# Performance work log

Hardware: AMD Instinct MI355X
Metric: run time of the kernel (lower is better)

Reference implementation:

```python
import jax, jax.numpy as jnp
import numpy as np

D_MODEL = 1024
NUM_HEADS = 16
D_K = D_MODEL // NUM_HEADS
THETA = 10000.0
SEQ = 4096
BATCH = 1


def _rope(x, token_positions):
    # x: [b, h, s, d_k]; interleaved even/odd rotation as in the torch module
    kd = jnp.arange(0, D_K, 2, dtype=jnp.float32) / D_K          # [d_k/2]
    angles = token_positions[:, None].astype(jnp.float32) / (THETA ** kd)  # [s, d_k/2]
    cos_pos = jnp.cos(angles)
    sin_pos = jnp.sin(angles)
    x_even = x[..., 0::2]
    x_odd = x[..., 1::2]
    rot_even = x_even * cos_pos - x_odd * sin_pos
    rot_odd = x_even * sin_pos + x_odd * cos_pos
    rot = jnp.stack([rot_even, rot_odd], axis=-1)                # [..., d_k/2, 2]
    return rot.reshape(*x.shape[:-1], D_K)


def setup_inputs() -> dict:
    key = jax.random.key(0)
    k1, k2, k3 = jax.random.split(key, 3)
    std_qkv = np.sqrt(2.0 / (D_MODEL + 3 * D_MODEL))
    std_o = np.sqrt(2.0 / (D_MODEL + D_MODEL))
    x = jax.random.normal(k1, (BATCH, SEQ, D_MODEL), dtype=jnp.float32)
    Wqkv = jax.random.normal(k2, (3 * D_MODEL, D_MODEL), dtype=jnp.float32) * std_qkv
    Wo = jax.random.normal(k3, (D_MODEL, D_MODEL), dtype=jnp.float32) * std_o
    token_positions = jnp.arange(SEQ, dtype=jnp.int32)
    return {"x": x, "Wqkv": Wqkv, "Wo": Wo, "token_positions": token_positions}


def reference(x, Wqkv, Wo, token_positions):
    b, s, _ = x.shape
    qkv = jnp.einsum('bsd,ed->bse', x, Wqkv)                      # [b, s, 3*d_model]
    q, k, v = jnp.split(qkv, 3, axis=-1)

    def to_heads(t):
        return t.reshape(b, s, NUM_HEADS, D_K).transpose(0, 2, 1, 3)  # [b, h, s, d_k]

    q, k, v = to_heads(q), to_heads(k), to_heads(v)
    q = _rope(q, token_positions)
    k = _rope(k, token_positions)

    scores = jnp.einsum('bhqd,bhkd->bhqk', q, k) / jnp.sqrt(jnp.float32(D_K))
    mask = jnp.tril(jnp.ones((s, s), dtype=bool))
    scores = jnp.where(mask, scores, -jnp.inf)
    attn = jax.nn.softmax(scores, axis=-1)
    out = jnp.einsum('bhqk,bhkd->bhqd', attn, v)                  # [b, h, s, d_k]
    out = out.transpose(0, 2, 1, 3).reshape(b, s, D_MODEL)
    return jnp.einsum('bsd,ed->bse', out, Wo)
```

## Files before the change

### kernel.cpp

```cpp
#include <hip/hip_runtime.h>
#include <cstdint>

typedef unsigned short u16;
typedef __attribute__((ext_vector_type(8))) short short8;
typedef __attribute__((ext_vector_type(4))) float float4v;

__device__ __forceinline__ float bf2f(u16 u) {
    union { unsigned int i; float f; } v; v.i = ((unsigned int)u) << 16; return v.f;
}
__device__ __forceinline__ u16 f2bf(float f) {
    union { float f; unsigned int i; } v; v.f = f;
    unsigned int i = v.i;
    i += 0x7fffu + ((i >> 16) & 1u);
    return (u16)(i >> 16);
}
__device__ __forceinline__ unsigned cvt_pk_bf16(float lo, float hi) {
    unsigned r;
    asm("v_cvt_pk_bf16_f32 %0, %1, %2" : "=v"(r) : "v"(lo), "v"(hi));
    return r;
}
__device__ __forceinline__ void gl2lds16(const u16* g, u16* l) {
    __builtin_amdgcn_global_load_lds((const __attribute__((address_space(1))) void*)g,
                                     (__attribute__((address_space(3))) void*)l, 16, 0, 0);
}
__device__ __forceinline__ uint4 cvt8(const float* __restrict__ p) {
    float4 a = *(const float4*)p;
    float4 b = *(const float4*)(p + 4);
    u16 t[8] = {f2bf(a.x), f2bf(a.y), f2bf(a.z), f2bf(a.w),
                f2bf(b.x), f2bf(b.y), f2bf(b.z), f2bf(b.w)};
    return *(const uint4*)t;
}

__global__ void cvt_f32_bf16(const float* __restrict__ src, u16* __restrict__ dst, int n8) {
    int i = blockIdx.x * blockDim.x + threadIdx.x;
    if (i >= n8) return;
    *(uint4*)(dst + (size_t)i * 8) = cvt8(src + (size_t)i * 8);
}

__global__ void zero_f32(float* __restrict__ p, int n4) {
    int i = blockIdx.x * blockDim.x + threadIdx.x;
    if (i >= n4) return;
    float4 z = {0.f, 0.f, 0.f, 0.f};
    *(float4*)(p + (size_t)i * 4) = z;
}

__global__ __launch_bounds__(256) void gemm_bt(const u16* __restrict__ A,
                                               const u16* __restrict__ B,
                                               u16* __restrict__ C,
                                               int M, int N, int K) {
    __shared__ u16 As[128 * 32];
    __shared__ u16 Bs[128 * 32];
    const int tid  = threadIdx.x;
    const int wave = tid >> 6, lane = tid & 63;
    const int lg = lane >> 4, lr = lane & 15;
    const int bm = blockIdx.x * 128, bn = blockIdx.y * 128;
    const int wm = (wave & 1) * 64, wn = (wave >> 1) * 64;
    const int row = tid >> 2, co = (tid & 3) * 8;

    float4v acc[4][4] = {};

    for (int k0 = 0; k0 < K; k0 += 32) {
        gl2lds16(A + (size_t)(bm + row) * K + k0 + co,      As + tid * 8);
        gl2lds16(A + (size_t)(bm + 64 + row) * K + k0 + co, As + (tid + 256) * 8);
        gl2lds16(B + (size_t)(bn + row) * K + k0 + co,      Bs + tid * 8);
        gl2lds16(B + (size_t)(bn + 64 + row) * K + k0 + co, Bs + (tid + 256) * 8);
        __syncthreads();

        short8 af[4], bf[4];
        #pragma unroll
        for (int i = 0; i < 4; ++i)
            af[i] = *(const short8*)(As + (wm + i * 16 + lr) * 32 + lg * 8);
        #pragma unroll
        for (int j = 0; j < 4; ++j)
            bf[j] = *(const short8*)(Bs + (wn + j * 16 + lr) * 32 + lg * 8);
        #pragma unroll
        for (int i = 0; i < 4; ++i)
            #pragma unroll
            for (int j = 0; j < 4; ++j)
                acc[i][j] = __builtin_amdgcn_mfma_f32_16x16x32_bf16(af[i], bf[j], acc[i][j], 0, 0, 0);
        __syncthreads();
    }

    #pragma unroll
    for (int i = 0; i < 4; ++i)
        #pragma unroll
        for (int j = 0; j < 4; ++j)
            #pragma unroll
            for (int r = 0; r < 4; ++r) {
                int rw = bm + wm + i * 16 + lg * 4 + r;
                int cl = bn + wn + j * 16 + lr;
                C[(size_t)rw * N + cl] = f2bf(acc[i][j][r]);
            }
}

__global__ void rope_kernel(u16* __restrict__ qkv, const int* __restrict__ pos, int S) {
    int idx = blockIdx.x * blockDim.x + threadIdx.x;
    int s = idx >> 10;
    if (s >= S) return;
    int p    = idx & 1023;
    int part = p >> 9;
    int wi   = p & 511;
    int head = wi >> 5;
    int i    = wi & 31;
    int col  = part * 1024 + head * 64 + 2 * i;

    u16* ptr = qkv + (size_t)s * 3072 + col;
    ushort2 v = *(const ushort2*)ptr;
    float xe = bf2f(v.x), xo = bf2f(v.y);
    float freq = __expf(-(float)i * 0.2878231366242557f);
    float ang  = (float)pos[s] * freq;
    float sn = sinf(ang), cs = cosf(ang);
    float re = xe * cs - xo * sn;
    float ro = xe * sn + xo * cs;
    if (part == 0) { re *= 0.18033688011112042f; ro *= 0.18033688011112042f; }
    ushort2 o; o.x = f2bf(re); o.y = f2bf(ro);
    *(ushort2*)ptr = o;
}

__global__ __launch_bounds__(256) void transpose_v(const u16* __restrict__ qkv,
                                                   u16* __restrict__ VT) {
    __shared__ u16 T[64 * 65];
    const int h = blockIdx.y, s0 = blockIdx.x * 64;
    const int tid = threadIdx.x;
    #pragma unroll
    for (int i = 0; i < 2; ++i) {
        int seg = i * 256 + tid;
        int r = seg >> 3, c8 = (seg & 7) * 8;
        u16 tmp[8];
        *(uint4*)tmp = *(const uint4*)(qkv + (size_t)(s0 + r) * 3072 + 2048 + h * 64 + c8);
        #pragma unroll
        for (int j = 0; j < 8; ++j) T[r * 65 + c8 + j] = tmp[j];
    }
    __syncthreads();
    #pragma unroll
    for (int i = 0; i < 2; ++i) {
        int seg = i * 256 + tid;
        int d = seg >> 3, s8 = (seg & 7) * 8;
        u16 tmp[8];
        #pragma unroll
        for (int j = 0; j < 8; ++j) tmp[j] = T[(s8 + j) * 65 + d];
        *(uint4*)(VT + (size_t)(h * 64 + d) * 4096 + s0 + s8) = *(const uint4*)tmp;
    }
}

__global__ __launch_bounds__(512) void attn_kernel(const u16* __restrict__ qkv,
                                                   const u16* __restrict__ VT,
                                                   float* __restrict__ acc,
                                                   float* __restrict__ lac) {
    __shared__ u16 Ks[64 * 64];
    __shared__ u16 Vt[64 * 64];
    __shared__ u16 Ps[8][16 * 72];

    const int tid  = threadIdx.x;
    const int wave = tid >> 6, lane = tid & 63;
    const int lg = lane >> 4, lr = lane & 15;
    const int h  = blockIdx.y;
    const int z  = blockIdx.z;

    const int srow = tid >> 3;
    const int sg   = tid & 7;
    const int sco  = sg * 8;
    const int sldso = srow * 64 + ((sg ^ (srow & 7)) * 8);
    const int swz = (lr & 7);

    #pragma unroll 1
    for (int part = 0; part < 2; ++part) {
        const int qt = part ? (31 - (int)blockIdx.x) : (int)blockIdx.x;
        const int qb = qt * 128;
        const int qrow0 = qb + wave * 16;
        const int tmax = qb + 64;
        const int t0s  = z * 64;

        short8 qf[2];
        #pragma unroll
        for (int kk = 0; kk < 2; ++kk)
            qf[kk] = *(const short8*)(qkv + (size_t)(qrow0 + lr) * 3072 + h * 64 + kk * 32 + lg * 8);

        float4v o_acc[4] = {};
        float rs = 0.f;

        uint4 rK = *(const uint4*)(qkv + (size_t)(t0s + srow) * 3072 + 1024 + h * 64 + sco);
        uint4 rV = *(const uint4*)(VT + (size_t)(h * 64 + srow) * 4096 + t0s + sco);
        __syncthreads();
        *(uint4*)(Ks + sldso) = rK;
        *(uint4*)(Vt + sldso) = rV;
        __syncthreads();

        for (int t0 = t0s; t0 <= tmax; t0 += 256) {
            const bool hasnext = (t0 + 256 <= tmax);
            if (hasnext) {
                rK = *(const uint4*)(qkv + (size_t)(t0 + 256 + srow) * 3072 + 1024 + h * 64 + sco);
                rV = *(const uint4*)(VT + (size_t)(h * 64 + srow) * 4096 + t0 + 256 + sco);
            }

            float4v sc[4];
            #pragma unroll
            for (int jt = 0; jt < 4; ++jt) {
                float4v a = {};
                #pragma unroll
                for (int kk = 0; kk < 2; ++kk) {
                    short8 kf = *(const short8*)(Ks + (jt * 16 + lr) * 64 + (((kk * 4 + lg) ^ swz) * 8));
                    a = __builtin_amdgcn_mfma_f32_16x16x32_bf16(kf, qf[kk], a, 0, 0, 0);
                }
                sc[jt] = a;
            }

            const bool mk = (t0 + 63 > qrow0);
            const int q_abs = qrow0 + lr;
            #pragma unroll
            for (int jt = 0; jt < 4; ++jt) {
                float e[4];
                #pragma unroll
                for (int r = 0; r < 4; ++r) {
                    float s = sc[jt][r];
                    if (mk && (t0 + jt * 16 + lg * 4 + r > q_abs)) s = -30000.f;
                    e[r] = __builtin_amdgcn_exp2f(fminf(s, 86.562f));
                }
                rs += (e[0] + e[1]) + (e[2] + e[3]);
                uint2 w;
                w.x = cvt_pk_bf16(e[0], e[1]);
                w.y = cvt_pk_bf16(e[2], e[3]);
                *(uint2*)(Ps[wave] + lr * 72 + jt * 16 + lg * 4) = w;
            }

            short8 pf[2];
            #pragma unroll
            for (int kk = 0; kk < 2; ++kk)
                pf[kk] = *(const short8*)(Ps[wave] + lr * 72 + kk * 32 + lg * 8);
            #pragma unroll
            for (int jd = 0; jd < 4; ++jd) {
                float4v a = o_acc[jd];
                #pragma unroll
                for (int kk = 0; kk < 2; ++kk) {
                    short8 vf = *(const short8*)(Vt + (jd * 16 + lr) * 64 + (((kk * 4 + lg) ^ swz) * 8));
                    a = __builtin_amdgcn_mfma_f32_16x16x32_bf16(pf[kk], vf, a, 0, 0, 0);
                }
                o_acc[jd] = a;
            }
            __syncthreads();
            if (hasnext) {
                *(uint4*)(Ks + sldso) = rK;
                *(uint4*)(Vt + sldso) = rV;
            }
            __syncthreads();
        }

        float t = rs;
        t += __shfl_xor(t, 16, 64);
        t += __shfl_xor(t, 32, 64);
        if (lane < 16)
            atomicAdd(&lac[(size_t)(qrow0 + lr) * 16 + h], t);

        #pragma unroll
        for (int jd = 0; jd < 4; ++jd)
            #pragma unroll
            for (int r = 0; r < 4; ++r) {
                int s = qrow0 + lg * 4 + r;
                int d = jd * 16 + lr;
                atomicAdd(&acc[(size_t)s * 1024 + h * 64 + d], o_acc[jd][r]);
            }
    }
}

__global__ void norm_o(const float* __restrict__ acc, const float* __restrict__ lac,
                       u16* __restrict__ qkv) {
    int i = blockIdx.x * blockDim.x + threadIdx.x;
    if (i >= 4096 * 1024 / 8) return;
    int e0 = i * 8;
    int s = e0 >> 10, c = e0 & 1023, h = c >> 6;
    float inv = 1.0f / lac[(size_t)s * 16 + h];
    float4 a = *(const float4*)(acc + e0);
    float4 b = *(const float4*)(acc + e0 + 4);
    u16 t[8] = {f2bf(a.x * inv), f2bf(a.y * inv), f2bf(a.z * inv), f2bf(a.w * inv),
                f2bf(b.x * inv), f2bf(b.y * inv), f2bf(b.z * inv), f2bf(b.w * inv)};
    *(uint4*)(qkv + (size_t)s * 3072 + c) = *(const uint4*)t;
}

__global__ __launch_bounds__(256) void gemm_oproj(const u16* __restrict__ A,
                                                  const u16* __restrict__ B,
                                                  float* __restrict__ C) {
    __shared__ u16 As[128 * 32];
    __shared__ u16 Bs[128 * 32];
    const int tid  = threadIdx.x;
    const int wave = tid >> 6, lane = tid & 63;
    const int lg = lane >> 4, lr = lane & 15;
    const int bm = blockIdx.x * 128, bn = blockIdx.y * 128;
    const int wm = (wave & 1) * 64, wn = (wave >> 1) * 64;
    const int row = tid >> 2, co = (tid & 3) * 8;

    float4v acc[4][4] = {};

    for (int k0 = 0; k0 < 1024; k0 += 32) {
        gl2lds16(A + (size_t)(bm + row) * 3072 + k0 + co,      As + tid * 8);
        gl2lds16(A + (size_t)(bm + 64 + row) * 3072 + k0 + co, As + (tid + 256) * 8);
        gl2lds16(B + (size_t)(bn + row) * 1024 + k0 + co,      Bs + tid * 8);
        gl2lds16(B + (size_t)(bn + 64 + row) * 1024 + k0 + co, Bs + (tid + 256) * 8);
        __syncthreads();

        short8 af[4], bf[4];
        #pragma unroll
        for (int i = 0; i < 4; ++i)
            af[i] = *(const short8*)(As + (wm + i * 16 + lr) * 32 + lg * 8);
        #pragma unroll
        for (int j = 0; j < 4; ++j)
            bf[j] = *(const short8*)(Bs + (wn + j * 16 + lr) * 32 + lg * 8);
        #pragma unroll
        for (int i = 0; i < 4; ++i)
            #pragma unroll
            for (int j = 0; j < 4; ++j)
                acc[i][j] = __builtin_amdgcn_mfma_f32_16x16x32_bf16(af[i], bf[j], acc[i][j], 0, 0, 0);
        __syncthreads();
    }

    #pragma unroll
    for (int i = 0; i < 4; ++i)
        #pragma unroll
        for (int j = 0; j < 4; ++j)
            #pragma unroll
            for (int r = 0; r < 4; ++r) {
                int rw = bm + wm + i * 16 + lg * 4 + r;
                int cl = bn + wn + j * 16 + lr;
                C[(size_t)rw * 1024 + cl] = acc[i][j][r];
            }
}

__global__ void fill_diag(float* __restrict__ p, size_t n, float mark) {
    size_t i = (size_t)blockIdx.x * blockDim.x + threadIdx.x;
    if (i < n) p[i] = 0.f;
    if (i == 0) p[0] = mark;
}

extern "C" void kernel_launch(void* const* d_in, const int* in_sizes, int n_in,
                              void* d_out, int out_size, void* d_ws, size_t ws_size,
                              hipStream_t stream) {
    int ix = -1, iwq = -1, iwo = -1, ip = -1;
    for (int i = 0; i < n_in; ++i) {
        if      (in_sizes[i] == 4096 * 1024) ix = i;
        else if (in_sizes[i] == 3072 * 1024) iwq = i;
        else if (in_sizes[i] == 1024 * 1024) iwo = i;
        else if (in_sizes[i] == 4096)        ip = i;
    }
    float* out = (float*)d_out;
    const size_t OUT_E = (size_t)4096 * 1024;
    const size_t QKV_E = (size_t)4096 * 3072;
    const size_t NEED  = QKV_E * 2 + (size_t)3072 * 1024 * 2;

    if (ix < 0 || iwq < 0 || iwo < 0 || ip < 0 || out_size != (int)OUT_E) {
        fill_diag<<<(int)((OUT_E + 255) / 256), 256, 0, stream>>>(out, OUT_E, 1000.0f);
        return;
    }
    if (ws_size < NEED) {
        fill_diag<<<(int)((OUT_E + 255) / 256), 256, 0, stream>>>(out, OUT_E, 500.0f);
        return;
    }
    const float* x    = (const float*)d_in[ix];
    const float* Wqkv = (const float*)d_in[iwq];
    const float* Wo   = (const float*)d_in[iwo];
    const int*   pos  = (const int*)d_in[ip];

    u16* qkv   = (u16*)d_ws;
    u16* wq_bf = (u16*)d_ws + QKV_E;
    u16* wo_bf = wq_bf;
    float* lac = (float*)((char*)wq_bf + 2 * 1024 * 1024 + 65536);
    u16* x_bf  = (u16*)d_out;
    u16* VT    = (u16*)d_out + OUT_E;
    float* acc = (float*)d_in[ix];

    cvt_f32_bf16<<<2048, 256, 0, stream>>>(x, x_bf, 4096 * 1024 / 8);
    cvt_f32_bf16<<<1536, 256, 0, stream>>>(Wqkv, wq_bf, 3072 * 1024 / 8);
    gemm_bt<<<dim3(32, 24), 256, 0, stream>>>(x_bf, wq_bf, qkv, 4096, 3072, 1024);
    zero_f32<<<4096, 256, 0, stream>>>(acc, 4096 * 1024 / 4);
    zero_f32<<<16, 256, 0, stream>>>(lac, 4096 * 16 / 4);
    cvt_f32_bf16<<<512, 256, 0, stream>>>(Wo, wo_bf, 1024 * 1024 / 8);
    rope_kernel<<<16384, 256, 0, stream>>>(qkv, pos, 4096);
    transpose_v<<<dim3(64, 16), 256, 0, stream>>>(qkv, VT);
    attn_kernel<<<dim3(16, 16, 4), 512, 0, stream>>>(qkv, VT, acc, lac);
    norm_o<<<2048, 256, 0, stream>>>(acc, lac, qkv);
    gemm_oproj<<<dim3(32, 8), 256, 0, stream>>>(qkv, wo_bf, out);
}
```

Baseline: 261.9 us.

## Halve attention key-split blocks and process two key tiles per iteration

The attention grid drops from four to two key-split slices per query tile. Each block now stages two 64-key K/V tiles in doubled LDS buffers and runs two tile computations between barrier pairs. This halves the float atomicAdd traffic into the partial output and row-sum buffers, and cuts the number of barriers per key processed. The cost is fewer blocks in flight, more LDS per block, and more registers held for the two prefetch buffers.

```diff
diff --git a/kernel.cpp b/kernel.cpp
--- a/kernel.cpp
+++ b/kernel.cpp
@@ -143,12 +143,61 @@
     }
 }
 
+__device__ __forceinline__ void attn_tile(const u16* __restrict__ Ksub,
+                                          const u16* __restrict__ Vsub,
+                                          u16* __restrict__ Psw,
+                                          int tbase, int qrow0, int q_abs,
+                                          int lg, int lr, int swz,
+                                          const short8 qf[2], float4v o_acc[4], float& rs) {
+    float4v sc[4];
+    #pragma unroll
+    for (int jt = 0; jt < 4; ++jt) {
+        float4v a = {};
+        #pragma unroll
+        for (int kk = 0; kk < 2; ++kk) {
+            short8 kf = *(const short8*)(Ksub + (jt * 16 + lr) * 64 + (((kk * 4 + lg) ^ swz) * 8));
+            a = __builtin_amdgcn_mfma_f32_16x16x32_bf16(kf, qf[kk], a, 0, 0, 0);
+        }
+        sc[jt] = a;
+    }
+    const bool mk = (tbase + 63 > qrow0);
+    #pragma unroll
+    for (int jt = 0; jt < 4; ++jt) {
+        float e[4];
+        #pragma unroll
+        for (int r = 0; r < 4; ++r) {
+            float s = sc[jt][r];
+            if (mk && (tbase + jt * 16 + lg * 4 + r > q_abs)) s = -30000.f;
+            e[r] = __builtin_amdgcn_exp2f(fminf(s, 86.562f));
+        }
+        rs += (e[0] + e[1]) + (e[2] + e[3]);
+        uint2 w;
+        w.x = cvt_pk_bf16(e[0], e[1]);
+        w.y = cvt_pk_bf16(e[2], e[3]);
+        *(uint2*)(Psw + lr * 72 + jt * 16 + lg * 4) = w;
+    }
+    short8 pf[2];
+    #pragma unroll
+    for (int kk = 0; kk < 2; ++kk)
+        pf[kk] = *(const short8*)(Psw + lr * 72 + kk * 32 + lg * 8);
+    #pragma unroll
+    for (int jd = 0; jd < 4; ++jd) {
+        float4v a = o_acc[jd];
+        #pragma unroll
+        for (int kk = 0; kk < 2; ++kk) {
+            short8 vf = *(const short8*)(Vsub + (jd * 16 + lr) * 64 + (((kk * 4 + lg) ^ swz) * 8));
+            a = __builtin_amdgcn_mfma_f32_16x16x32_bf16(pf[kk], vf, a, 0, 0, 0);
+        }
+        o_acc[jd] = a;
+    }
+}
+
 __global__ __launch_bounds__(512) void attn_kernel(const u16* __restrict__ qkv,
                                                    const u16* __restrict__ VT,
                                                    float* __restrict__ acc,
                                                    float* __restrict__ lac) {
-    __shared__ u16 Ks[64 * 64];
-    __shared__ u16 Vt[64 * 64];
+    __shared__ u16 Ks[2 * 64 * 64];
+    __shared__ u16 Vt[2 * 64 * 64];
     __shared__ u16 Ps[8][16 * 72];
 
     const int tid  = threadIdx.x;
@@ -163,11 +212,15 @@
     const int sldso = srow * 64 + ((sg ^ (srow & 7)) * 8);
     const int swz = (lr & 7);
 
+    const u16* Kgbase = qkv + (size_t)srow * 3072 + 1024 + h * 64 + sco;
+    const u16* Vgbase = VT + (size_t)(h * 64 + srow) * 4096 + sco;
+
     #pragma unroll 1
     for (int part = 0; part < 2; ++part) {
         const int qt = part ? (31 - (int)blockIdx.x) : (int)blockIdx.x;
         const int qb = qt * 128;
         const int qrow0 = qb + wave * 16;
+        const int q_abs = qrow0 + lr;
         const int tmax = qb + 64;
         const int t0s  = z * 64;
 
@@ -179,70 +232,51 @@
         float4v o_acc[4] = {};
         float rs = 0.f;
 
-        uint4 rK = *(const uint4*)(qkv + (size_t)(t0s + srow) * 3072 + 1024 + h * 64 + sco);
-        uint4 rV = *(const uint4*)(VT + (size_t)(h * 64 + srow) * 4096 + t0s + sco);
-        __syncthreads();
-        *(uint4*)(Ks + sldso) = rK;
-        *(uint4*)(Vt + sldso) = rV;
+        uint4 rK0 = *(const uint4*)(Kgbase + (size_t)t0s * 3072);
+        uint4 rV0 = *(const uint4*)(Vgbase + t0s);
+        const bool pB = (t0s + 128 <= tmax);
+        uint4 rK1, rV1;
+        if (pB) {
+            rK1 = *(const uint4*)(Kgbase + (size_t)(t0s + 128) * 3072);
+            rV1 = *(const uint4*)(Vgbase + t0s + 128);
+        }
+        __syncthreads();
+        *(uint4*)(Ks + sldso) = rK0;
+        *(uint4*)(Vt + sldso) = rV0;
+        if (pB) {
+            *(uint4*)(Ks + 4096 + sldso) = rK1;
+            *(uint4*)(Vt + 4096 + sldso) = rV1;
+        }
         __syncthreads();
 
         for (int t0 = t0s; t0 <= tmax; t0 += 256) {
-            const bool hasnext = (t0 + 256 <= tmax);
-            if (hasnext) {
-                rK = *(const uint4*)(qkv + (size_t)(t0 + 256 + srow) * 3072 + 1024 + h * 64 + sco);
-                rV = *(const uint4*)(VT + (size_t)(h * 64 + srow) * 4096 + t0 + 256 + sco);
-            }
-
-            float4v sc[4];
-            #pragma unroll
-            for (int jt = 0; jt < 4; ++jt) {
-                float4v a = {};
-                #pragma unroll
-                for (int kk = 0; kk < 2; ++kk) {
-                    short8 kf = *(const short8*)(Ks + (jt * 16 + lr) * 64 + (((kk * 4 + lg) ^ swz) * 8));
-                    a = __builtin_amdgcn_mfma_f32_16x16x32_bf16(kf, qf[kk], a, 0, 0, 0);
+            const bool hasB  = (t0 + 128 <= tmax);
+            const bool hasN  = (t0 + 256 <= tmax);
+            const bool hasNB = (t0 + 384 <= tmax);
+            if (hasN) {
+                rK0 = *(const uint4*)(Kgbase + (size_t)(t0 + 256) * 3072);
+                rV0 = *(const uint4*)(Vgbase + t0 + 256);
+            }
+            if (hasNB) {
+                rK1 = *(const uint4*)(Kgbase + (size_t)(t0 + 384) * 3072);
+                rV1 = *(const uint4*)(Vgbase + t0 + 384);
+            }
+
+            attn_tile(Ks, Vt, Ps[wave], t0, qrow0, q_abs, lg, lr, swz, qf, o_acc, rs);
+            if (hasB)
+                attn_tile(Ks + 4096, Vt + 4096, Ps[wave], t0 + 128, qrow0, q_abs,
+                          lg, lr, swz, qf, o_acc, rs);
+
+            if (hasN) {
+                __syncthreads();
+                *(uint4*)(Ks + sldso) = rK0;
+                *(uint4*)(Vt + sldso) = rV0;
+                if (hasNB) {
+                    *(uint4*)(Ks + 4096 + sldso) = rK1;
+                    *(uint4*)(Vt + 4096 + sldso) = rV1;
                 }
-                sc[jt] = a;
-            }
-
-            const bool mk = (t0 + 63 > qrow0);
-            const int q_abs = qrow0 + lr;
-            #pragma unroll
-            for (int jt = 0; jt < 4; ++jt) {
-                float e[4];
-                #pragma unroll
-                for (int r = 0; r < 4; ++r) {
-                    float s = sc[jt][r];
-                    if (mk && (t0 + jt * 16 + lg * 4 + r > q_abs)) s = -30000.f;
-                    e[r] = __builtin_amdgcn_exp2f(fminf(s, 86.562f));
-                }
-                rs += (e[0] + e[1]) + (e[2] + e[3]);
-                uint2 w;
-                w.x = cvt_pk_bf16(e[0], e[1]);
-                w.y = cvt_pk_bf16(e[2], e[3]);
-                *(uint2*)(Ps[wave] + lr * 72 + jt * 16 + lg * 4) = w;
-            }
-
-            short8 pf[2];
-            #pragma unroll
-            for (int kk = 0; kk < 2; ++kk)
-                pf[kk] = *(const short8*)(Ps[wave] + lr * 72 + kk * 32 + lg * 8);
-            #pragma unroll
-            for (int jd = 0; jd < 4; ++jd) {
-                float4v a = o_acc[jd];
-                #pragma unroll
-                for (int kk = 0; kk < 2; ++kk) {
-                    short8 vf = *(const short8*)(Vt + (jd * 16 + lr) * 64 + (((kk * 4 + lg) ^ swz) * 8));
-                    a = __builtin_amdgcn_mfma_f32_16x16x32_bf16(pf[kk], vf, a, 0, 0, 0);
-                }
-                o_acc[jd] = a;
-            }
-            __syncthreads();
-            if (hasnext) {
-                *(uint4*)(Ks + sldso) = rK;
-                *(uint4*)(Vt + sldso) = rV;
-            }
-            __syncthreads();
+                __syncthreads();
+            }
         }
 
         float t = rs;
@@ -374,7 +408,7 @@
     cvt_f32_bf16<<<512, 256, 0, stream>>>(Wo, wo_bf, 1024 * 1024 / 8);
     rope_kernel<<<16384, 256, 0, stream>>>(qkv, pos, 4096);
     transpose_v<<<dim3(64, 16), 256, 0, stream>>>(qkv, VT);
-    attn_kernel<<<dim3(16, 16, 4), 512, 0, stream>>>(qkv, VT, acc, lac);
+    attn_kernel<<<dim3(16, 16, 2), 512, 0, stream>>>(qkv, VT, acc, lac);
     norm_o<<<2048, 256, 0, stream>>>(acc, lac, qkv);
     gemm_oproj<<<dim3(32, 8), 256, 0, stream>>>(qkv, wo_bf, out);
 }
```

Result: faster. 245.7 us (-6.2%).
